# Optimization experiments

Hardware: AMD Instinct MI355X
Metric: run time of the kernel (lower is better)

The kernel has to match this reference:

```python
import jax, jax.numpy as jnp
import numpy as np

NUM_QUBITS = 4
NUM_LAYERS = 3
C64 = jnp.complex64


def _apply_1q(state, U, axis):
    """Apply a single-qubit gate. state: (M,2,2,2,2); U: (2,2) shared or (M,2,2) per-batch."""
    s = jnp.moveaxis(state, axis, -1)
    if U.ndim == 2:
        s = jnp.einsum('...b,ab->...a', s, U)
    else:
        s = jnp.einsum('m...b,mab->m...a', s, U)
    return jnp.moveaxis(s, -1, axis)


def _apply_cnot(state, c_axis, t_axis):
    """CNOT: flip target amplitudes where control bit == 1."""
    s0 = jax.lax.index_in_dim(state, 0, axis=c_axis, keepdims=True)
    s1 = jax.lax.index_in_dim(state, 1, axis=c_axis, keepdims=True)
    s1 = jnp.flip(s1, axis=t_axis)
    return jnp.concatenate([s0, s1], axis=c_axis)


def _rx_mat(theta):
    """theta: (M,) -> (M,2,2) RX matrices."""
    c = jnp.cos(theta / 2).astype(C64)
    s = (-1j * jnp.sin(theta / 2)).astype(C64)
    row0 = jnp.stack([c, s], axis=-1)
    row1 = jnp.stack([s, c], axis=-1)
    return jnp.stack([row0, row1], axis=-2)


def _rot_mat(phi, theta, omega):
    """PennyLane Rot(phi,theta,omega) = RZ(omega) RY(theta) RZ(phi) -> (2,2)."""
    c = jnp.cos(theta / 2).astype(C64)
    s = jnp.sin(theta / 2).astype(C64)
    m00 = jnp.exp(-0.5j * (phi + omega).astype(C64)) * c
    m01 = -jnp.exp(0.5j * (phi - omega).astype(C64)) * s
    m10 = jnp.exp(-0.5j * (phi - omega).astype(C64)) * s
    m11 = jnp.exp(0.5j * (phi + omega).astype(C64)) * c
    return jnp.stack([jnp.stack([m00, m01]), jnp.stack([m10, m11])])


def setup_inputs() -> dict:
    key = jax.random.key(0)
    k1, k2 = jax.random.split(key)
    x = jax.random.normal(k1, (256, 4096, 4), dtype=jnp.float32)
    params = jax.random.normal(k2, (NUM_LAYERS, NUM_QUBITS, 3), dtype=jnp.float32) * 0.1
    return {"x": x, "params": params}


def reference(x, params):
    B, N, _ = x.shape
    M = B * N
    angles = x.reshape(M, NUM_QUBITS)

    # |0000> initial state, batched: (M, 2,2,2,2)
    state = jnp.zeros((M, 16), dtype=C64).at[:, 0].set(1.0)
    state = state.reshape((M,) + (2,) * NUM_QUBITS)

    # data-encoding RX layer (per-patch angles)
    for q in range(NUM_QUBITS):
        state = _apply_1q(state, _rx_mat(angles[:, q]), 1 + q)

    # variational layers: Rot on every qubit, then CNOT chain
    for l in range(NUM_LAYERS):
        for q in range(NUM_QUBITS):
            U = _rot_mat(params[l, q, 0], params[l, q, 1], params[l, q, 2])
            state = _apply_1q(state, U, 1 + q)
        for q in range(NUM_QUBITS - 1):
            state = _apply_cnot(state, 1 + q, 2 + q)

    # <Z_q> = P(bit_q=0) - P(bit_q=1)
    probs = state.real ** 2 + state.imag ** 2  # (M,2,2,2,2)
    zs = []
    for q in range(NUM_QUBITS):
        p = jnp.moveaxis(probs, 1 + q, 1)
        zs.append(jnp.sum(p[:, 0] - p[:, 1], axis=(1, 2, 3)))
    return jnp.stack(zs, axis=-1).reshape(B, N, NUM_QUBITS)
```

## Files before the change

### kernel.cpp

```cpp
#include <hip/hip_runtime.h>

__global__ __launch_bounds__(256) void qprecomp(const float* __restrict__ params,
                                                float* __restrict__ C) {
  __shared__ float colR[16][16];
  __shared__ float colI[16][16];
  __shared__ float Um[12][8];
  __shared__ float4 S4[256];
  const int t = threadIdx.x;

  if (t < 16) {
#pragma unroll
    for (int i = 0; i < 16; ++i) { colR[t][i] = 0.0f; colI[t][i] = 0.0f; }
    int pc = __popc(t) & 3;
    colR[t][t] = (pc == 0) ? 1.0f : (pc == 2 ? -1.0f : 0.0f);
    colI[t][t] = (pc == 1) ? -1.0f : (pc == 3 ? 1.0f : 0.0f);
  }
  if (t < 12) {
    float phi = params[t * 3 + 0], th = params[t * 3 + 1], om = params[t * 3 + 2];
    float sa, ca, sb, cb, s2, c2;
    __sincosf(0.5f * (phi + om), &sa, &ca);
    __sincosf(0.5f * (phi - om), &sb, &cb);
    __sincosf(0.5f * th, &s2, &c2);
    Um[t][0] =  c2 * ca; Um[t][1] = -c2 * sa;
    Um[t][2] = -s2 * cb; Um[t][3] = -s2 * sb;
    Um[t][4] =  s2 * cb; Um[t][5] = -s2 * sb;
    Um[t][6] =  c2 * ca; Um[t][7] =  c2 * sa;
  }
  __syncthreads();

  const int j = t >> 3, p = t & 7;
  for (int l = 0; l < 3; ++l) {
    for (int q = 0; q < 4; ++q) {
      if (t < 128) {
        const int g = l * 4 + q;
        const int B = 3 - q, mask = 1 << B;
        const int i0 = ((p >> B) << (B + 1)) | (p & (mask - 1));
        const int i1 = i0 | mask;
        float a0r = colR[j][i0], a0i = colI[j][i0];
        float a1r = colR[j][i1], a1i = colI[j][i1];
        float m00r = Um[g][0], m00i = Um[g][1], m01r = Um[g][2], m01i = Um[g][3];
        float m10r = Um[g][4], m10i = Um[g][5], m11r = Um[g][6], m11i = Um[g][7];
        colR[j][i0] = m00r * a0r - m00i * a0i + m01r * a1r - m01i * a1i;
        colI[j][i0] = m00r * a0i + m00i * a0r + m01r * a1i + m01i * a1r;
        colR[j][i1] = m10r * a0r - m10i * a0i + m11r * a1r - m11i * a1i;
        colI[j][i1] = m10r * a0i + m10i * a0r + m11r * a1i + m11i * a1r;
      }
      __syncthreads();
    }
    for (int q = 0; q < 3; ++q) {
      if (t < 64) {
        const int jj = t >> 2, pp = t & 3;
        const int Bc = 3 - q, Bt = 2 - q;
        int fps[2], nf = 0;
        for (int b = 0; b < 4; ++b)
          if (b != Bc && b != Bt) fps[nf++] = b;
        const int i  = (1 << Bc) | ((pp & 1) << fps[0]) | (((pp >> 1) & 1) << fps[1]);
        const int i2 = i | (1 << Bt);
        float tr = colR[jj][i], ti = colI[jj][i];
        colR[jj][i] = colR[jj][i2]; colI[jj][i] = colI[jj][i2];
        colR[jj][i2] = tr;          colI[jj][i2] = ti;
      }
      __syncthreads();
    }
  }

  {
    const int jj = t >> 4, k = t & 15;
    float s0 = 0.f, s1 = 0.f, s2 = 0.f, s3 = 0.f;
#pragma unroll
    for (int i = 0; i < 16; ++i) {
      float pr = colR[jj][i] * colR[k][i] + colI[jj][i] * colI[k][i];
      s0 += ((i >> 3) & 1) ? -pr : pr;
      s1 += ((i >> 2) & 1) ? -pr : pr;
      s2 += ((i >> 1) & 1) ? -pr : pr;
      s3 += ( i       & 1) ? -pr : pr;
    }
    S4[t] = make_float4(s0, s1, s2, s3);
  }
  __syncthreads();

  if (t < 81) {
    const int m[4] = { t / 27, (t / 9) % 3, (t / 3) % 3, t % 3 };
    float a0 = 0.f, a1 = 0.f, a2 = 0.f, a3 = 0.f;
    for (int c = 0; c < 16; ++c) {
      int jj = 0, kk = 0; bool ok = true;
      for (int q = 0; q < 4; ++q) {
        int jb, kb;
        if (m[q] == 1) { jb = (c >> q) & 1; kb = 1 - jb; }
        else { jb = kb = (m[q] >> 1); if ((c >> q) & 1) ok = false; }
        jj |= jb << (3 - q); kk |= kb << (3 - q);
      }
      if (!ok) continue;
      float4 sv = S4[jj * 16 + kk];
      a0 += sv.x; a1 += sv.y; a2 += sv.z; a3 += sv.w;
    }
    C[t * 4 + 0] = a0 * 0.0625f;
    C[t * 4 + 1] = a1 * 0.0625f;
    C[t * 4 + 2] = a2 * 0.0625f;
    C[t * 4 + 3] = a3 * 0.0625f;
  }
}

__device__ __forceinline__ void build_t(const float4 a, float* t01, float* t23) {
  float s0, c0, s1, c1, s2, c2, s3, c3;
  __sincosf(a.x, &s0, &c0);
  __sincosf(a.y, &s1, &c1);
  __sincosf(a.z, &s2, &c2);
  __sincosf(a.w, &s3, &c3);
  float w0[3] = { 1.0f + c0, s0, 1.0f - c0 };
  float w1[3] = { 1.0f + c1, s1, 1.0f - c1 };
  float w2[3] = { 1.0f + c2, s2, 1.0f - c2 };
  float w3[3] = { 1.0f + c3, s3, 1.0f - c3 };
#pragma unroll
  for (int i = 0; i < 3; ++i)
#pragma unroll
    for (int jj = 0; jj < 3; ++jj) {
      t01[i * 3 + jj] = w0[i] * w1[jj];
      t23[i * 3 + jj] = w2[i] * w3[jj];
    }
}

__global__ __launch_bounds__(256) void qmain(const float4* __restrict__ x4,
                                             const float4* __restrict__ C4,
                                             float4* __restrict__ out,
                                             int half) {
  const int gid = blockIdx.x * 256 + threadIdx.x;
  float tA01[9], tA23[9], tB01[9], tB23[9];
  build_t(x4[gid], tA01, tA23);
  build_t(x4[gid + half], tB01, tB23);

  float zA0 = 0.f, zA1 = 0.f, zA2 = 0.f, zA3 = 0.f;
  float zB0 = 0.f, zB1 = 0.f, zB2 = 0.f, zB3 = 0.f;
#pragma unroll
  for (int a = 0; a < 9; ++a) {
#pragma unroll
    for (int b = 0; b < 9; ++b) {
      const float4 c = C4[a * 9 + b];
      const float pA = tA01[a] * tA23[b];
      const float pB = tB01[a] * tB23[b];
      zA0 = fmaf(c.x, pA, zA0); zA1 = fmaf(c.y, pA, zA1);
      zA2 = fmaf(c.z, pA, zA2); zA3 = fmaf(c.w, pA, zA3);
      zB0 = fmaf(c.x, pB, zB0); zB1 = fmaf(c.y, pB, zB1);
      zB2 = fmaf(c.z, pB, zB2); zB3 = fmaf(c.w, pB, zB3);
    }
  }
  out[gid]        = make_float4(zA0, zA1, zA2, zA3);
  out[gid + half] = make_float4(zB0, zB1, zB2, zB3);
}

extern "C" void kernel_launch(void* const* d_in, const int* in_sizes, int n_in,
                              void* d_out, int out_size, void* d_ws, size_t ws_size,
                              hipStream_t stream) {
  const float* x      = (const float*)d_in[0];
  const float* params = (const float*)d_in[1];
  float* C = (float*)d_ws;

  qprecomp<<<1, 256, 0, stream>>>(params, C);

  const int M    = in_sizes[0] / 4;
  const int half = M / 2;
  const int blocks = half / 256;
  qmain<<<blocks, 256, 0, stream>>>((const float4*)x, (const float4*)C,
                                    (float4*)d_out, half);
}
```

Measured before the change: 22.98 us.

## Compute circuit unitary columns in registers per thread in the single-block precompute

```diff
diff --git a/kernel.cpp b/kernel.cpp
--- a/kernel.cpp
+++ b/kernel.cpp
@@ -1,89 +1,97 @@
 #include <hip/hip_runtime.h>
 
-__global__ __launch_bounds__(256) void qprecomp(const float* __restrict__ params,
-                                                float* __restrict__ C) {
+__global__ __launch_bounds__(64) void qprecomp(const float* __restrict__ params,
+                                               float* __restrict__ C) {
   __shared__ float colR[16][16];
   __shared__ float colI[16][16];
-  __shared__ float Um[12][8];
   __shared__ float4 S4[256];
   const int t = threadIdx.x;
 
+  float uR[16], uI[16];
+  {
+    const int pc = __popc(t) & 3;
+    const float dre = (pc == 0) ? 1.0f : (pc == 2 ? -1.0f : 0.0f);
+    const float dim = (pc == 1) ? -1.0f : (pc == 3 ? 1.0f : 0.0f);
+#pragma unroll
+    for (int i = 0; i < 16; ++i) {
+      uR[i] = (i == t) ? dre : 0.0f;
+      uI[i] = (i == t) ? dim : 0.0f;
+    }
+  }
+
+#pragma unroll
+  for (int l = 0; l < 3; ++l) {
+#pragma unroll
+    for (int q = 0; q < 4; ++q) {
+      const int g = l * 4 + q;
+      const float phi = params[g * 3 + 0];
+      const float th  = params[g * 3 + 1];
+      const float om  = params[g * 3 + 2];
+      const float sa = __sinf(0.5f * (phi + om)), ca = __cosf(0.5f * (phi + om));
+      const float sb = __sinf(0.5f * (phi - om)), cb = __cosf(0.5f * (phi - om));
+      const float s2 = __sinf(0.5f * th),         c2 = __cosf(0.5f * th);
+      const float m00r =  c2 * ca, m00i = -c2 * sa;
+      const float m01r = -s2 * cb, m01i = -s2 * sb;
+      const float m10r =  s2 * cb, m10i = -s2 * sb;
+      const float m11r =  c2 * ca, m11i =  c2 * sa;
+      const int B = 3 - q;
+#pragma unroll
+      for (int p = 0; p < 8; ++p) {
+        const int i0 = ((p >> B) << (B + 1)) | (p & ((1 << B) - 1));
+        const int i1 = i0 | (1 << B);
+        const float a0r = uR[i0], a0i = uI[i0];
+        const float a1r = uR[i1], a1i = uI[i1];
+        uR[i0] = m00r * a0r - m00i * a0i + m01r * a1r - m01i * a1i;
+        uI[i0] = m00r * a0i + m00i * a0r + m01r * a1i + m01i * a1r;
+        uR[i1] = m10r * a0r - m10i * a0i + m11r * a1r - m11i * a1i;
+        uI[i1] = m10r * a0i + m10i * a0r + m11r * a1i + m11i * a1r;
+      }
+    }
+#pragma unroll
+    for (int q = 0; q < 3; ++q) {
+      const int Bc = 3 - q, Bt = 2 - q;
+#pragma unroll
+      for (int i = 0; i < 16; ++i) {
+        if ((((i >> Bc) & 1) == 1) && (((i >> Bt) & 1) == 0)) {
+          const int i2 = i | (1 << Bt);
+          const float tr = uR[i], ti = uI[i];
+          uR[i] = uR[i2]; uI[i] = uI[i2];
+          uR[i2] = tr;    uI[i2] = ti;
+        }
+      }
+    }
+  }
+
   if (t < 16) {
 #pragma unroll
-    for (int i = 0; i < 16; ++i) { colR[t][i] = 0.0f; colI[t][i] = 0.0f; }
-    int pc = __popc(t) & 3;
-    colR[t][t] = (pc == 0) ? 1.0f : (pc == 2 ? -1.0f : 0.0f);
-    colI[t][t] = (pc == 1) ? -1.0f : (pc == 3 ? 1.0f : 0.0f);
-  }
-  if (t < 12) {
-    float phi = params[t * 3 + 0], th = params[t * 3 + 1], om = params[t * 3 + 2];
-    float sa, ca, sb, cb, s2, c2;
-    __sincosf(0.5f * (phi + om), &sa, &ca);
-    __sincosf(0.5f * (phi - om), &sb, &cb);
-    __sincosf(0.5f * th, &s2, &c2);
-    Um[t][0] =  c2 * ca; Um[t][1] = -c2 * sa;
-    Um[t][2] = -s2 * cb; Um[t][3] = -s2 * sb;
-    Um[t][4] =  s2 * cb; Um[t][5] = -s2 * sb;
-    Um[t][6] =  c2 * ca; Um[t][7] =  c2 * sa;
+    for (int i = 0; i < 16; ++i) { colR[t][i] = uR[i]; colI[t][i] = uI[i]; }
   }
   __syncthreads();
 
-  const int j = t >> 3, p = t & 7;
-  for (int l = 0; l < 3; ++l) {
-    for (int q = 0; q < 4; ++q) {
-      if (t < 128) {
-        const int g = l * 4 + q;
-        const int B = 3 - q, mask = 1 << B;
-        const int i0 = ((p >> B) << (B + 1)) | (p & (mask - 1));
-        const int i1 = i0 | mask;
-        float a0r = colR[j][i0], a0i = colI[j][i0];
-        float a1r = colR[j][i1], a1i = colI[j][i1];
-        float m00r = Um[g][0], m00i = Um[g][1], m01r = Um[g][2], m01i = Um[g][3];
-        float m10r = Um[g][4], m10i = Um[g][5], m11r = Um[g][6], m11i = Um[g][7];
-        colR[j][i0] = m00r * a0r - m00i * a0i + m01r * a1r - m01i * a1i;
-        colI[j][i0] = m00r * a0i + m00i * a0r + m01r * a1i + m01i * a1r;
-        colR[j][i1] = m10r * a0r - m10i * a0i + m11r * a1r - m11i * a1i;
-        colI[j][i1] = m10r * a0i + m10i * a0r + m11r * a1i + m11i * a1r;
-      }
-      __syncthreads();
-    }
-    for (int q = 0; q < 3; ++q) {
-      if (t < 64) {
-        const int jj = t >> 2, pp = t & 3;
-        const int Bc = 3 - q, Bt = 2 - q;
-        int fps[2], nf = 0;
-        for (int b = 0; b < 4; ++b)
-          if (b != Bc && b != Bt) fps[nf++] = b;
-        const int i  = (1 << Bc) | ((pp & 1) << fps[0]) | (((pp >> 1) & 1) << fps[1]);
-        const int i2 = i | (1 << Bt);
-        float tr = colR[jj][i], ti = colI[jj][i];
-        colR[jj][i] = colR[jj][i2]; colI[jj][i] = colI[jj][i2];
-        colR[jj][i2] = tr;          colI[jj][i2] = ti;
-      }
-      __syncthreads();
-    }
-  }
-
-  {
-    const int jj = t >> 4, k = t & 15;
+#pragma unroll
+  for (int it = 0; it < 4; ++it) {
+    const int pp = t + it * 64;
+    const int jj = pp >> 4, k = pp & 15;
     float s0 = 0.f, s1 = 0.f, s2 = 0.f, s3 = 0.f;
 #pragma unroll
     for (int i = 0; i < 16; ++i) {
-      float pr = colR[jj][i] * colR[k][i] + colI[jj][i] * colI[k][i];
+      const float pr = colR[jj][i] * colR[k][i] + colI[jj][i] * colI[k][i];
       s0 += ((i >> 3) & 1) ? -pr : pr;
       s1 += ((i >> 2) & 1) ? -pr : pr;
       s2 += ((i >> 1) & 1) ? -pr : pr;
       s3 += ( i       & 1) ? -pr : pr;
     }
-    S4[t] = make_float4(s0, s1, s2, s3);
+    S4[pp] = make_float4(s0, s1, s2, s3);
   }
   __syncthreads();
 
-  if (t < 81) {
-    const int m[4] = { t / 27, (t / 9) % 3, (t / 3) % 3, t % 3 };
+  for (int bin = t; bin < 81; bin += 64) {
+    const int m0 = bin / 27, m1 = (bin / 9) % 3, m2 = (bin / 3) % 3, m3 = bin % 3;
+    const int m[4] = { m0, m1, m2, m3 };
     float a0 = 0.f, a1 = 0.f, a2 = 0.f, a3 = 0.f;
     for (int c = 0; c < 16; ++c) {
       int jj = 0, kk = 0; bool ok = true;
+#pragma unroll
       for (int q = 0; q < 4; ++q) {
         int jb, kb;
         if (m[q] == 1) { jb = (c >> q) & 1; kb = 1 - jb; }
@@ -91,26 +99,25 @@
         jj |= jb << (3 - q); kk |= kb << (3 - q);
       }
       if (!ok) continue;
-      float4 sv = S4[jj * 16 + kk];
+      const float4 sv = S4[jj * 16 + kk];
       a0 += sv.x; a1 += sv.y; a2 += sv.z; a3 += sv.w;
     }
-    C[t * 4 + 0] = a0 * 0.0625f;
-    C[t * 4 + 1] = a1 * 0.0625f;
-    C[t * 4 + 2] = a2 * 0.0625f;
-    C[t * 4 + 3] = a3 * 0.0625f;
+    C[bin * 4 + 0] = a0 * 0.0625f;
+    C[bin * 4 + 1] = a1 * 0.0625f;
+    C[bin * 4 + 2] = a2 * 0.0625f;
+    C[bin * 4 + 3] = a3 * 0.0625f;
   }
 }
 
 __device__ __forceinline__ void build_t(const float4 a, float* t01, float* t23) {
-  float s0, c0, s1, c1, s2, c2, s3, c3;
-  __sincosf(a.x, &s0, &c0);
-  __sincosf(a.y, &s1, &c1);
-  __sincosf(a.z, &s2, &c2);
-  __sincosf(a.w, &s3, &c3);
-  float w0[3] = { 1.0f + c0, s0, 1.0f - c0 };
-  float w1[3] = { 1.0f + c1, s1, 1.0f - c1 };
-  float w2[3] = { 1.0f + c2, s2, 1.0f - c2 };
-  float w3[3] = { 1.0f + c3, s3, 1.0f - c3 };
+  const float s0 = __sinf(a.x), c0 = __cosf(a.x);
+  const float s1 = __sinf(a.y), c1 = __cosf(a.y);
+  const float s2 = __sinf(a.z), c2 = __cosf(a.z);
+  const float s3 = __sinf(a.w), c3 = __cosf(a.w);
+  const float w0[3] = { 1.0f + c0, s0, 1.0f - c0 };
+  const float w1[3] = { 1.0f + c1, s1, 1.0f - c1 };
+  const float w2[3] = { 1.0f + c2, s2, 1.0f - c2 };
+  const float w3[3] = { 1.0f + c3, s3, 1.0f - c3 };
 #pragma unroll
   for (int i = 0; i < 3; ++i)
 #pragma unroll
@@ -120,7 +127,7 @@
     }
 }
 
-__global__ __launch_bounds__(256) void qmain(const float4* __restrict__ x4,
+__global__ __launch_bounds__(256) void qeval(const float4* __restrict__ x4,
                                              const float4* __restrict__ C4,
                                              float4* __restrict__ out,
                                              int half) {
@@ -155,11 +162,11 @@
   const float* params = (const float*)d_in[1];
   float* C = (float*)d_ws;
 
-  qprecomp<<<1, 256, 0, stream>>>(params, C);
+  qprecomp<<<1, 64, 0, stream>>>(params, C);
 
-  const int M    = in_sizes[0] / 4;
-  const int half = M / 2;
+  const int M      = in_sizes[0] / 4;
+  const int half   = M / 2;
   const int blocks = half / 256;
-  qmain<<<blocks, 256, 0, stream>>>((const float4*)x, (const float4*)C,
+  qeval<<<blocks, 256, 0, stream>>>((const float4*)x, (const float4*)C,
                                     (float4*)d_out, half);
 }
```

New measurement: 28.31 us. +23.2%, slower.
